# Optimization experiments

Measured on AMD Instinct MI355X. Metric: run time of the kernel, lower is better.

## Reference

```python
import jax, jax.numpy as jnp
import numpy as np

N, K, C_S, C_Z, C_G, H, NUM_RBF = 768, 32, 384, 128, 16, 4, 64
E = N * K
DH = C_Z // H  # 32
LN_EPS = 1e-5
DIST_EPS = 1e-8


def _rbf(D, D_min=0.0, D_max=20.0, D_count=NUM_RBF):
    # Gaussian radial basis expansion (GVP/ProteinMPNN style)
    mu = jnp.linspace(D_min, D_max, D_count, dtype=D.dtype)
    sigma = (D_max - D_min) / D_count
    return jnp.exp(-(((D[..., None] - mu) / sigma) ** 2))


def setup_inputs() -> dict:
    key = jax.random.key(0)
    ks = jax.random.split(key, 24)
    node_features = jax.random.normal(ks[0], (N, C_S), dtype=jnp.float32)
    node_trans = jax.random.uniform(ks[1], (N, 3), dtype=jnp.float32) * 30.0  # coords in a 30A box
    edge_features = jax.random.normal(ks[2], (E, C_Z), dtype=jnp.float32)
    src = jax.random.randint(ks[3], (E,), 0, N)
    dst = jnp.repeat(jnp.arange(N), K)  # sorted-by-destination layout (assume_sorted)
    edge_index = jnp.stack([src, dst]).astype(jnp.int64)

    def lin(k, fan_in, fan_out, scale=0.02):
        return jax.random.normal(k, (fan_in, fan_out), dtype=jnp.float32) * scale

    return {
        "node_features": node_features,
        "node_trans": node_trans,
        "edge_features": edge_features,
        "edge_index": edge_index,
        "w_left": lin(ks[4], C_S, C_G), "b_left": jnp.zeros((C_G,), jnp.float32),
        "w_right": lin(ks[5], C_S, C_G), "b_right": jnp.zeros((C_G,), jnp.float32),
        "w_bgate": lin(ks[6], C_G * C_G, C_Z), "b_bgate": jnp.zeros((C_Z,), jnp.float32),
        "w_dist": lin(ks[7], NUM_RBF, C_Z), "b_dist": jnp.zeros((C_Z,), jnp.float32),
        "w_tobias": lin(ks[8], C_Z, H),
        "ln_g": jnp.ones((C_Z,), jnp.float32), "ln_b": jnp.zeros((C_Z,), jnp.float32),
        "w_q": lin(ks[9], C_Z, C_Z), "b_q": jnp.zeros((C_Z,), jnp.float32),
        "w_kv": lin(ks[10], C_Z, 2 * C_Z), "b_kv": jnp.zeros((2 * C_Z,), jnp.float32),
        "w_out": lin(ks[11], C_Z, C_Z), "b_out": jnp.zeros((C_Z,), jnp.float32),
        "w_ogate": lin(ks[12], C_Z, C_Z), "b_ogate": jnp.zeros((C_Z,), jnp.float32),
    }


def reference(node_features, node_trans, edge_features, edge_index,
              w_left, b_left, w_right, b_right, w_bgate, b_bgate,
              w_dist, b_dist, w_tobias, ln_g, ln_b,
              w_q, b_q, w_kv, b_kv, w_out, b_out, w_ogate, b_ogate):
    # sparse -> knn graph (edges pre-sorted by destination, exactly K per node)
    knn_idx = edge_index[0].reshape(N, K)            # [N, K] source node of each neighbor edge
    feat = edge_features.reshape(N, K, C_Z)          # [N, K, c_z]

    # LayerNorm over c_z
    mu = feat.mean(-1, keepdims=True)
    var = feat.var(-1, keepdims=True)
    z = (feat - mu) * jax.lax.rsqrt(var + LN_EPS) * ln_g + ln_b  # [N, K, c_z]

    # outer-product gating bias
    nl = node_features @ w_left + b_left             # [N, c_gate_s]
    nr = node_features @ w_right + b_right
    e1 = nl[knn_idx]                                 # [N, K, c_gate_s]
    e2 = nr[knn_idx]
    edge3 = jnp.einsum('nik,njl->nijkl', e1, e2).reshape(N, K, K, C_G * C_G)
    gate = edge3 @ w_bgate + b_bgate                 # [N, K, K, c_z]

    # RBF distance bias
    t = node_trans[knn_idx]                          # [N, K, 3]
    diff = t[:, :, None, :] - t[:, None, :, :] + DIST_EPS
    dist = jnp.sqrt(jnp.sum(diff * diff, axis=-1))   # [N, K, K]
    db = _rbf(dist) @ w_dist + b_dist                # [N, K, K, c_z]
    bias = (jax.nn.sigmoid(gate) * db) @ w_tobias    # [N, K, K, H]

    # attention over the K neighbors of each node
    q = (z @ w_q + b_q).reshape(N, K, H, DH)
    kv = z @ w_kv + b_kv
    k_ = kv[..., :C_Z].reshape(N, K, H, DH)
    v = kv[..., C_Z:].reshape(N, K, H, DH)
    scores = jnp.einsum('nihd,njhd->nhij', q, k_) / jnp.sqrt(jnp.asarray(DH, q.dtype))
    scores = scores + bias.transpose(0, 3, 1, 2)     # [N, H, K, K] (mask all-True -> no -inf term)
    p = jax.nn.softmax(scores, axis=-1)
    o = jnp.einsum('nhij,njhd->nihd', p, v).reshape(N, K, C_Z)

    # output gate + projection, then knn -> sparse (identity reshape: full mask, sorted edges)
    o = o * jax.nn.sigmoid(z @ w_ogate + b_ogate)
    out = (o @ w_out + b_out).reshape(E, C_Z)
    return out
```

## Files before the change

### kernel.cpp

```cpp
#include <hip/hip_runtime.h>

#define NN   768
#define KKN  32
#define CS   384
#define CZ   128
#define CG   16
#define NH   4
#define DHD  32
#define NRBF 64
#define EE   (NN*KKN)

#define RBF_STEP    (20.0f/63.0f)
#define RBF_INVSTEP (63.0f/20.0f)
#define RBF_INVSIG  3.2f
#define RBF_SI      (RBF_STEP*RBF_INVSIG)

typedef __attribute__((ext_vector_type(8))) short bf16x8;
typedef __attribute__((ext_vector_type(4))) float f32x4;

__device__ __forceinline__ float bfl(unsigned int u){ return __uint_as_float(u << 16); }
__device__ __forceinline__ float bfh(unsigned int u){ return __uint_as_float(u & 0xFFFF0000u); }
__device__ __forceinline__ unsigned int packbf(float a, float b){
  unsigned int r;
  asm("v_cvt_pk_bf16_f32 %0, %1, %2" : "=v"(r) : "v"(a), "v"(b));
  return r;
}
__device__ __forceinline__ float fastrcp(float x){
  float r;
  asm("v_rcp_f32 %0, %1" : "=v"(r) : "v"(x));
  return r;
}
__device__ __forceinline__ float sigm(float x){ return fastrcp(1.0f + __expf(-x)); }

__global__ __launch_bounds__(256) void k1_pre(
    const float* __restrict__ nf, const float* __restrict__ ef,
    const float* __restrict__ wl, const float* __restrict__ bl,
    const float* __restrict__ wr, const float* __restrict__ br,
    const float* __restrict__ lng, const float* __restrict__ lnb,
    float* __restrict__ nlw, float* __restrict__ nrw,
    unsigned short* __restrict__ zw,
    const float* __restrict__ wq, const float* __restrict__ wkv,
    const float* __restrict__ wog, const float* __restrict__ wout,
    const float* __restrict__ wd, const float* __restrict__ wt,
    const float* __restrict__ wb, const float* __restrict__ bgf,
    unsigned short* __restrict__ wqkvogT, unsigned short* __restrict__ woutT,
    unsigned short* __restrict__ wdT, unsigned short* __restrict__ wtT,
    unsigned short* __restrict__ wbP, unsigned short* __restrict__ bgP)
{
  int b = blockIdx.x, t = threadIdx.x;
  if (b < 1536){
    int rl = t >> 4, l16 = t & 15;
    size_t e = (size_t)b*16 + rl;
    const float4* row = (const float4*)(ef + e*CZ);
    float4 x0 = row[l16*2], x1 = row[l16*2+1];
    float v[8] = {x0.x,x0.y,x0.z,x0.w,x1.x,x1.y,x1.z,x1.w};
    float s = 0.f, q = 0.f;
    #pragma unroll
    for (int u=0;u<8;u++){ s += v[u]; q += v[u]*v[u]; }
    #pragma unroll
    for (int m=1;m<16;m<<=1){ s += __shfl_xor(s,m); q += __shfl_xor(q,m); }
    float mean = s*(1.f/128.f);
    float var  = q*(1.f/128.f) - mean*mean;
    float rs = rsqrtf(var + 1e-5f);
    int c0 = l16*8;
    unsigned int pk[4];
    #pragma unroll
    for (int u=0;u<4;u++){
      float z0 = (v[2*u]  -mean)*rs*lng[c0+2*u]   + lnb[c0+2*u];
      float z1 = (v[2*u+1]-mean)*rs*lng[c0+2*u+1] + lnb[c0+2*u+1];
      pk[u] = packbf(z0,z1);
    }
    ((uint4*)(zw + e*CZ))[l16] = make_uint4(pk[0],pk[1],pk[2],pk[3]);
  } else if (b < 2304){
    int blk2 = b - 1536;
    int seg = blk2 / 96;
    int within = blk2 - seg*96;
    int gid = within*256 + t;
    int side = (gid >= 12288) ? 1 : 0;
    int idx = gid - side*12288;
    int nd = idx >> 4, c = idx & 15;
    const float* w = side ? wr : wl;
    float acc = (seg==0) ? (side ? br[c] : bl[c]) : 0.f;
    const float* nrow = nf + (size_t)nd*CS;
    int kb = seg*48;
    #pragma unroll 4
    for (int k=kb;k<kb+48;k++) acc += nrow[k]*w[k*CG+c];
    atomicAdd((side? nrw : nlw)+idx, acc);
  } else {
    int id = (b - 2304)*256 + t;
    float v[8];
    if (id < 8192){
      int c = id & 511, g = id >> 9;
      const float* src; int ld, col;
      if (c < 128){ src = wq; ld = 128; col = c; }
      else if (c < 384){ src = wkv; ld = 256; col = c-128; }
      else { src = wog; ld = 128; col = c-384; }
      #pragma unroll
      for (int j=0;j<8;j++) v[j] = src[(size_t)(g*8+j)*ld + col];
      *(uint4*)(wqkvogT + c*128 + ((g + c)&15)*8) = make_uint4(
        packbf(v[0],v[1]),packbf(v[2],v[3]),packbf(v[4],v[5]),packbf(v[6],v[7]));
    } else if (id < 10240){
      int l = id - 8192; int c = l & 127, g = l >> 7;
      #pragma unroll
      for (int j=0;j<8;j++) v[j] = wout[(size_t)(g*8+j)*128 + c];
      *(uint4*)(woutT + c*128 + ((g + c)&15)*8) = make_uint4(
        packbf(v[0],v[1]),packbf(v[2],v[3]),packbf(v[4],v[5]),packbf(v[6],v[7]));
    } else if (id < 11392){
      int l = id - 10240; int c = l & 127, g = l >> 7;
      #pragma unroll
      for (int j=0;j<8;j++) v[j] = (g<8) ? wd[(size_t)(g*8+j)*128 + c] : 0.f;
      *(uint4*)(wdT + c*72 + g*8) = make_uint4(
        packbf(v[0],v[1]),packbf(v[2],v[3]),packbf(v[4],v[5]),packbf(v[6],v[7]));
    } else if (id < 11460){
      int l = id - 11392; int h = l / 17, g = l % 17;
      #pragma unroll
      for (int j=0;j<8;j++){ int cc = g*8+j; v[j] = (cc<128)? wt[cc*4 + h] : 0.f; }
      *(uint4*)(wtT + h*136 + g*8) = make_uint4(
        packbf(v[0],v[1]),packbf(v[2],v[3]),packbf(v[4],v[5]),packbf(v[6],v[7]));
    } else if (id < 15556){
      int l2 = id - 11460;
      int c = l2 >> 5, sl = l2 & 31;
      int kl0 = sl*8;
      #pragma unroll
      for (int j=0;j<8;j++) v[j] = wb[(size_t)(kl0+j)*128 + c];
      *(uint4*)(wbP + c*256 + kl0) = make_uint4(
        packbf(v[0],v[1]),packbf(v[2],v[3]),packbf(v[4],v[5]),packbf(v[6],v[7]));
    } else if (id < 15684){
      int c = id - 15556;
      *(uint4*)(bgP + c*8) = make_uint4(packbf(bgf[c], 0.f), 0u, 0u, 0u);
    }
  }
}

__global__ __launch_bounds__(256) void k1b_sprep(
    const float* __restrict__ nlw, const float* __restrict__ nrw,
    const unsigned short* __restrict__ wbP,
    unsigned short* __restrict__ S_all, unsigned short* __restrict__ nrb)
{
  int n = blockIdx.x, t = threadIdx.x;
  float e1[16];
  #pragma unroll
  for (int k=0;k<16;k++) e1[k] = nlw[n*CG + k];
  int c = t>>1, l0 = (t&1)*8;
  float S[8];
  #pragma unroll
  for (int u=0;u<8;u++) S[u]=0.f;
  const unsigned short* wrow = wbP + c*256 + l0;
  #pragma unroll 4
  for (int k=0;k<16;k++){
    uint4 wv = *(const uint4*)(wrow + k*16);
    float wf[8] = { bfl(wv.x), bfh(wv.x), bfl(wv.y), bfh(wv.y),
                    bfl(wv.z), bfh(wv.z), bfl(wv.w), bfh(wv.w) };
    float ev = e1[k];
    #pragma unroll
    for (int u=0;u<8;u++) S[u] = fmaf(ev, wf[u], S[u]);
  }
  *(uint4*)(S_all + (size_t)n*2048 + c*16 + l0) = make_uint4(
    packbf(S[0],S[1]), packbf(S[2],S[3]), packbf(S[4],S[5]), packbf(S[6],S[7]));
  if (t < 8){
    *(unsigned int*)(nrb + n*CG + 2*t) = packbf(nrw[n*CG + 2*t], nrw[n*CG + 2*t + 1]);
  }
}

__global__ __launch_bounds__(256,4) void k2_bias(
    const long long* __restrict__ eidx, const float* __restrict__ trans,
    const unsigned short* __restrict__ S_all, const unsigned short* __restrict__ nrb,
    const unsigned short* __restrict__ wdTg, const unsigned short* __restrict__ wtTg,
    const unsigned short* __restrict__ bgP, const float* __restrict__ bd,
    float* __restrict__ biasw)
{
  int n = blockIdx.x >> 3, chunk = blockIdx.x & 7;
  int i0 = chunk*4;
  int t = threadIdx.x;
  int wave = t>>6, lane = t&63, q = lane>>4, l15 = lane&15;

  __shared__ __align__(16) unsigned short rbfb[32*72];
  __shared__ __align__(16) unsigned short Xb  [32*136];
  __shared__ __align__(16) float t3s[32][4];
  __shared__ __align__(16) float dsm[4][32];
  __shared__ int srcs[32];

  f32x4 zero4 = {0.f,0.f,0.f,0.f};
  uint4 uz = make_uint4(0,0,0,0);

  if (t < 32) srcs[t] = (int)eidx[(size_t)n*KKN + t];
  __syncthreads();
  if (t < 32){ int s = srcs[t];
    t3s[t][0]=trans[s*3]; t3s[t][1]=trans[s*3+1]; t3s[t][2]=trans[s*3+2]; }
  uint4 wdf[2][2];
  #pragma unroll
  for (int mt=0;mt<2;mt++){
    #pragma unroll
    for (int ks=0;ks<2;ks++)
      wdf[mt][ks] = *(const uint4*)(wdTg + (wave*32+mt*16+l15)*72 + ks*32 + q*8);
  }
  uint4 wtf[4];
  #pragma unroll
  for (int ks=0;ks<4;ks++)
    wtf[ks] = *(const uint4*)(wtTg + (l15&3)*136 + ks*32 + q*8);
  uint4 aBias[2];
  #pragma unroll
  for (int mt=0;mt<2;mt++)
    aBias[mt] = (q == 2) ? *(const uint4*)(bgP + (wave*32+mt*16+l15)*8) : uz;
  uint4 bE[2];
  #pragma unroll
  for (int nt=0;nt<2;nt++){
    int jn = srcs[nt*16 + l15];
    bE[nt] = (q < 2) ? *(const uint4*)(nrb + jn*CG + q*8)
                     : (q == 2 ? make_uint4(0x3F80u,0u,0u,0u) : uz);
  }
  uint4 aS[2], aSn[2];
  {
    int s0 = srcs[i0];
    #pragma unroll
    for (int mt=0;mt<2;mt++)
      aS[mt] = (q < 2) ? *(const uint4*)(S_all + (size_t)s0*2048 + (wave*32+mt*16+l15)*16 + q*8)
                       : aBias[mt];
  }
  __syncthreads();
  if (t < 128){
    int ii=t>>5, j=t&31;
    float dx=t3s[i0+ii][0]-t3s[j][0]+1e-8f;
    float dy=t3s[i0+ii][1]-t3s[j][1]+1e-8f;
    float dz=t3s[i0+ii][2]-t3s[j][2]+1e-8f;
    dsm[ii][j]=sqrtf(dx*dx+dy*dy+dz*dz);
  }
  __syncthreads();

  int jr = t>>3, sl = t&7;
  int c0base = wave*32 + q*4;
  float4 bdv[2];
  #pragma unroll
  for (int mt=0;mt<2;mt++) bdv[mt] = *(const float4*)(bd + c0base + mt*16);

  #pragma unroll 1
  for (int ii=0; ii<4; ii++){
    {
      float dI = dsm[ii][jr]*RBF_INVSIG;
      float e[8];
      #pragma unroll
      for (int u=0;u<8;u++){
        float x = fmaf((float)(sl*8+u), -RBF_SI, dI);
        e[u] = __expf(-x*x);
      }
      *(uint4*)&rbfb[jr*72 + sl*8] = make_uint4(
        packbf(e[0],e[1]), packbf(e[2],e[3]), packbf(e[4],e[5]), packbf(e[6],e[7]));
    }
    if (ii < 3){
      int s_n = srcs[i0+ii+1];
      #pragma unroll
      for (int mt=0;mt<2;mt++)
        aSn[mt] = (q < 2) ? *(const uint4*)(S_all + (size_t)s_n*2048 + (wave*32+mt*16+l15)*16 + q*8)
                          : aBias[mt];
    }
    __syncthreads();

    f32x4 ga[2][2], da[2][2];
    #pragma unroll
    for(int a=0;a<2;a++){
      #pragma unroll
      for(int b2=0;b2<2;b2++){ ga[a][b2]=zero4; da[a][b2]=zero4; }
    }
    #pragma unroll
    for(int mt=0;mt<2;mt++){
      #pragma unroll
      for(int nt=0;nt<2;nt++)
        ga[mt][nt] = __builtin_amdgcn_mfma_f32_16x16x32_bf16(
          *(const bf16x8*)&aS[mt], *(const bf16x8*)&bE[nt], ga[mt][nt], 0,0,0);
    }
    #pragma unroll
    for(int ks=0;ks<2;ks++){
      bf16x8 bR[2];
      #pragma unroll
      for(int nt=0;nt<2;nt++) bR[nt] = *(const bf16x8*)&rbfb[(nt*16+l15)*72 + ks*32 + q*8];
      #pragma unroll
      for(int mt=0;mt<2;mt++){
        #pragma unroll
        for(int nt=0;nt<2;nt++)
          da[mt][nt] = __builtin_amdgcn_mfma_f32_16x16x32_bf16(
            *(const bf16x8*)&wdf[mt][ks], bR[nt], da[mt][nt], 0,0,0);
      }
    }
    #pragma unroll
    for(int mt=0;mt<2;mt++){
      int c0 = c0base + mt*16;
      float4 bv = bdv[mt];
      #pragma unroll
      for(int nt=0;nt<2;nt++){
        float x0 = fastrcp(1.f + __expf(-ga[mt][nt][0]))*(da[mt][nt][0]+bv.x);
        float x1 = fastrcp(1.f + __expf(-ga[mt][nt][1]))*(da[mt][nt][1]+bv.y);
        float x2 = fastrcp(1.f + __expf(-ga[mt][nt][2]))*(da[mt][nt][2]+bv.z);
        float x3 = fastrcp(1.f + __expf(-ga[mt][nt][3]))*(da[mt][nt][3]+bv.w);
        *(uint2*)&Xb[(nt*16+l15)*136 + c0] = make_uint2(packbf(x0,x1), packbf(x2,x3));
      }
    }
    __syncthreads();

    if (wave < 2){
      f32x4 bacc = {0.f,0.f,0.f,0.f};
      #pragma unroll
      for(int ks=0;ks<4;ks++){
        bf16x8 bX = *(const bf16x8*)&Xb[(wave*16+l15)*136 + ks*32 + q*8];
        bacc = __builtin_amdgcn_mfma_f32_16x16x32_bf16(*(const bf16x8*)&wtf[ks], bX, bacc, 0,0,0);
      }
      if (q==0){
        int j = wave*16 + l15;
        float* base = biasw + (((size_t)n*4)*32 + (i0+ii))*32 + j;
        base[0] = bacc[0]; base[1024] = bacc[1]; base[2048] = bacc[2]; base[3072] = bacc[3];
      }
    }
    aS[0] = aSn[0]; aS[1] = aSn[1];
  }
}

__global__ __launch_bounds__(256,4) void k3_attn(
    const unsigned short* __restrict__ zw, const float* __restrict__ biasw,
    const unsigned short* __restrict__ wqkvogT, const unsigned short* __restrict__ woutT,
    const float* __restrict__ bq, const float* __restrict__ bkv, const float* __restrict__ bog,
    const float* __restrict__ bout, float* __restrict__ out)
{
  int n = blockIdx.x, t = threadIdx.x;
  int w = t>>6, lane = t&63, q = lane>>4, l15 = lane&15;

  __shared__ __align__(16) char smem[40960];
  f32x4 zero4 = {0.f,0.f,0.f,0.f};

  bf16x8 zfr[2][4];
  #pragma unroll
  for (int nt=0;nt<2;nt++){
    const unsigned short* zr = zw + ((size_t)n*32 + nt*16 + l15)*128;
    #pragma unroll
    for (int ks=0;ks<4;ks++) zfr[nt][ks] = *(const bf16x8*)(zr + ks*32 + q*8);
  }
  const float* bb = biasw + (size_t)(n*4 + w)*1024;
  float bbv[2][4][2];
  #pragma unroll
  for (int mt=0;mt<2;mt++){
    #pragma unroll
    for (int rg=0;rg<4;rg++){
      int i = mt*16 + q*4 + rg;
      bbv[mt][rg][0] = bb[i*32 + l15];
      bbv[mt][rg][1] = bb[i*32 + 16 + l15];
    }
  }
  const float* bseg = (w==0)? bq : (w==1)? bkv : (w==2)? (bkv+128) : bog;

  for (int r=0;r<8;r++){
    float4 bv = *(const float4*)(bseg + r*16 + q*4);
    f32x4 acc0 = zero4, acc1 = zero4;
    int cg = w*128 + r*16 + l15;
    const unsigned short* wrow = wqkvogT + cg*128;
    #pragma unroll
    for (int ks=0;ks<4;ks++){
      bf16x8 af = *(const bf16x8*)(wrow + (((ks*4+q) + cg)&15)*8);
      acc0 = __builtin_amdgcn_mfma_f32_16x16x32_bf16(af, zfr[0][ks], acc0, 0,0,0);
      acc1 = __builtin_amdgcn_mfma_f32_16x16x32_bf16(af, zfr[1][ks], acc1, 0,0,0);
    }
    #pragma unroll
    for (int nt=0;nt<2;nt++){
      f32x4 a = nt? acc1 : acc0;
      float v0,v1,v2,v3;
      if (w==3){ v0=sigm(a[0]+bv.x); v1=sigm(a[1]+bv.y); v2=sigm(a[2]+bv.z); v3=sigm(a[3]+bv.w); }
      else     { v0=a[0]+bv.x; v1=a[1]+bv.y; v2=a[2]+bv.z; v3=a[3]+bv.w; }
      int i = nt*16 + l15;
      if (w==2){
        unsigned short* vt = (unsigned short*)(smem + 16384) + (r*16 + q*4)*32 + i;
        unsigned int u01 = packbf(v0,v1), u23 = packbf(v2,v3);
        vt[0]  = (unsigned short)u01;  vt[32] = (unsigned short)(u01>>16);
        vt[64] = (unsigned short)u23;  vt[96] = (unsigned short)(u23>>16);
      } else {
        int blk = ((r*2 + (q>>1)) + i) & 15;
        *(uint2*)(smem + w*8192 + i*256 + blk*16 + (q&1)*8) = make_uint2(packbf(v0,v1), packbf(v2,v3));
      }
    }
  }
  __syncthreads();

  f32x4 sc4[2][2];
  {
    uint4 aQ[2], bK[2];
    #pragma unroll
    for (int mt=0;mt<2;mt++){
      int row = mt*16 + l15;
      aQ[mt] = *(const uint4*)(smem + row*256 + (((w*4+q) + row)&15)*16);
    }
    #pragma unroll
    for (int nt=0;nt<2;nt++){
      int row = nt*16 + l15;
      bK[nt] = *(const uint4*)(smem + 8192 + row*256 + (((w*4+q) + row)&15)*16);
    }
    #pragma unroll
    for (int mt=0;mt<2;mt++){
      #pragma unroll
      for (int nt=0;nt<2;nt++)
        sc4[mt][nt] = __builtin_amdgcn_mfma_f32_16x16x32_bf16(
          *(const bf16x8*)&aQ[mt], *(const bf16x8*)&bK[nt], zero4, 0,0,0);
    }
  }
  float inv_[2][4];
  #pragma unroll
  for (int mt=0;mt<2;mt++){
    #pragma unroll
    for (int rg=0;rg<4;rg++){
      sc4[mt][0][rg] = fmaf(sc4[mt][0][rg], 0.17677669529663687f, bbv[mt][rg][0]);
      sc4[mt][1][rg] = fmaf(sc4[mt][1][rg], 0.17677669529663687f, bbv[mt][rg][1]);
      float m = fmaxf(sc4[mt][0][rg], sc4[mt][1][rg]);
      m = fmaxf(m, __shfl_xor(m,1));
      m = fmaxf(m, __shfl_xor(m,2));
      m = fmaxf(m, __shfl_xor(m,4));
      m = fmaxf(m, __shfl_xor(m,8));
      sc4[mt][0][rg] = __expf(sc4[mt][0][rg] - m);
      sc4[mt][1][rg] = __expf(sc4[mt][1][rg] - m);
      float s = sc4[mt][0][rg] + sc4[mt][1][rg];
      s += __shfl_xor(s,1); s += __shfl_xor(s,2);
      s += __shfl_xor(s,4); s += __shfl_xor(s,8);
      inv_[mt][rg] = fastrcp(s);
    }
  }
  unsigned short* Pl = (unsigned short*)(smem + 32768 + w*2048);
  #pragma unroll
  for (int mt=0;mt<2;mt++){
    #pragma unroll
    for (int nt=0;nt<2;nt++){
      unsigned int u01 = packbf(sc4[mt][nt][0], sc4[mt][nt][1]);
      unsigned int u23 = packbf(sc4[mt][nt][2], sc4[mt][nt][3]);
      unsigned short* pp = Pl + (mt*16 + q*4)*32 + nt*16 + l15;
      pp[0]  = (unsigned short)u01;  pp[32] = (unsigned short)(u01>>16);
      pp[64] = (unsigned short)u23;  pp[96] = (unsigned short)(u23>>16);
    }
  }
  __syncthreads();

  f32x4 ov[2][2];
  {
    uint4 aP[2], bV[2];
    #pragma unroll
    for (int mt=0;mt<2;mt++)
      aP[mt] = *(const uint4*)(Pl + (mt*16 + l15)*32 + q*8);
    #pragma unroll
    for (int nt2=0;nt2<2;nt2++)
      bV[nt2] = *(const uint4*)((unsigned short*)(smem + 16384) + (w*32 + nt2*16 + l15)*32 + q*8);
    #pragma unroll
    for (int mt=0;mt<2;mt++){
      #pragma unroll
      for (int nt2=0;nt2<2;nt2++)
        ov[mt][nt2] = __builtin_amdgcn_mfma_f32_16x16x32_bf16(
          *(const bf16x8*)&aP[mt], *(const bf16x8*)&bV[nt2], zero4, 0,0,0);
    }
  }
  #pragma unroll
  for (int mt=0;mt<2;mt++){
    #pragma unroll
    for (int nt2=0;nt2<2;nt2++){
      #pragma unroll
      for (int rg=0;rg<4;rg++){
        int i = mt*16 + q*4 + rg;
        int c = w*32 + nt2*16 + l15;
        int off = i*256 + (((c>>3) + i)&15)*16 + (c&7)*2;
        unsigned short gus = *(const unsigned short*)(smem + 24576 + off);
        float g = __uint_as_float(((unsigned int)gus) << 16);
        float yv = ov[mt][nt2][rg] * inv_[mt][rg] * g;
        *(unsigned short*)(smem + off) = (unsigned short)packbf(yv, yv);
      }
    }
  }
  __syncthreads();

  bf16x8 yfr[2][4];
  #pragma unroll
  for (int mt=0;mt<2;mt++){
    int row = mt*16 + l15;
    #pragma unroll
    for (int ks=0;ks<4;ks++)
      yfr[mt][ks] = *(const bf16x8*)(smem + row*256 + (((ks*4+q) + row)&15)*16);
  }
  #pragma unroll
  for (int r2=0;r2<2;r2++){
    int c0 = (r2*4 + w)*16;
    int cg2 = c0 + l15;
    const unsigned short* orow = woutT + cg2*128;
    f32x4 oa0 = zero4, oa1 = zero4;
    #pragma unroll
    for (int ks=0;ks<4;ks++){
      bf16x8 bf = *(const bf16x8*)(orow + (((ks*4+q) + cg2)&15)*8);
      oa0 = __builtin_amdgcn_mfma_f32_16x16x32_bf16(yfr[0][ks], bf, oa0, 0,0,0);
      oa1 = __builtin_amdgcn_mfma_f32_16x16x32_bf16(yfr[1][ks], bf, oa1, 0,0,0);
    }
    float bov = bout[cg2];
    #pragma unroll
    for (int mt=0;mt<2;mt++){
      f32x4 oa = mt? oa1 : oa0;
      #pragma unroll
      for (int rg=0; rg<4; rg++){
        int i = mt*16 + q*4 + rg;
        out[((size_t)n*32 + i)*128 + cg2] = oa[rg] + bov;
      }
    }
  }
}

extern "C" void kernel_launch(void* const* d_in, const int* in_sizes, int n_in,
                              void* d_out, int out_size, void* d_ws, size_t ws_size,
                              hipStream_t stream)
{
  const float* nf  = (const float*)d_in[0];
  const float* tr  = (const float*)d_in[1];
  const float* ef  = (const float*)d_in[2];
  const long long* ei = (const long long*)d_in[3];
  const float* wl  = (const float*)d_in[4];  const float* bl  = (const float*)d_in[5];
  const float* wr  = (const float*)d_in[6];  const float* br  = (const float*)d_in[7];
  const float* wbg = (const float*)d_in[8];  const float* bbg = (const float*)d_in[9];
  const float* wdi = (const float*)d_in[10]; const float* bdi = (const float*)d_in[11];
  const float* wtb = (const float*)d_in[12];
  const float* lng = (const float*)d_in[13]; const float* lnb = (const float*)d_in[14];
  const float* wq  = (const float*)d_in[15]; const float* bq  = (const float*)d_in[16];
  const float* wkv = (const float*)d_in[17]; const float* bkv = (const float*)d_in[18];
  const float* wo  = (const float*)d_in[19]; const float* bo  = (const float*)d_in[20];
  const float* wog = (const float*)d_in[21]; const float* bog = (const float*)d_in[22];
  float* outp = (float*)d_out;
  float* ws = (float*)d_ws;
  float* nlw = ws;
  float* nrw = ws + 12288;
  float* biasw = ws + 24576;
  unsigned short* zw      = (unsigned short*)(ws + 3170304);
  unsigned short* wqkvogT = (unsigned short*)(ws + 4743168);
  unsigned short* woutT   = (unsigned short*)(ws + 4775936);
  unsigned short* wdTg    = (unsigned short*)(ws + 4784128);
  unsigned short* wtTg    = (unsigned short*)(ws + 4788736);
  unsigned short* bgPg    = wtTg + 544;
  unsigned short* wbPg    = (unsigned short*)(ws + 4789824);
  unsigned short* S_all   = (unsigned short*)(ws + 4806208);
  unsigned short* nrb     = (unsigned short*)(ws + 5592640);

  hipMemsetAsync(nlw, 0, 24576*sizeof(float), stream);
  hipLaunchKernelGGL(k1_pre, dim3(2366), dim3(256), 0, stream,
                     nf, ef, wl, bl, wr, br, lng, lnb, nlw, nrw, zw,
                     wq, wkv, wog, wo, wdi, wtb, wbg, bbg,
                     wqkvogT, woutT, wdTg, wtTg, wbPg, bgPg);
  hipLaunchKernelGGL(k1b_sprep, dim3(768), dim3(256), 0, stream,
                     nlw, nrw, wbPg, S_all, nrb);
  hipLaunchKernelGGL(k2_bias, dim3(6144), dim3(256), 0, stream,
                     ei, tr, S_all, nrb, wdTg, wtTg, bgPg, bdi, biasw);
  hipLaunchKernelGGL(k3_attn, dim3(768), dim3(256), 0, stream,
                     zw, biasw, wqkvogT, woutT, bq, bkv, bog, bo, outp);
}
```

Baseline: 192.9 us.

## Fuse bias computation kernel into attention kernel, keep bias in shared memory

```diff
diff --git a/kernel.cpp b/kernel.cpp
--- a/kernel.cpp
+++ b/kernel.cpp
@@ -162,23 +162,27 @@
   }
 }
 
-__global__ __launch_bounds__(256,4) void k2_bias(
+__global__ __launch_bounds__(256,4) void k23_fused(
     const long long* __restrict__ eidx, const float* __restrict__ trans,
     const unsigned short* __restrict__ S_all, const unsigned short* __restrict__ nrb,
     const unsigned short* __restrict__ wdTg, const unsigned short* __restrict__ wtTg,
     const unsigned short* __restrict__ bgP, const float* __restrict__ bd,
-    float* __restrict__ biasw)
+    const unsigned short* __restrict__ zw,
+    const unsigned short* __restrict__ wqkvogT, const unsigned short* __restrict__ woutT,
+    const float* __restrict__ bq, const float* __restrict__ bkv, const float* __restrict__ bog,
+    const float* __restrict__ bout, float* __restrict__ out)
 {
-  int n = blockIdx.x >> 3, chunk = blockIdx.x & 7;
-  int i0 = chunk*4;
-  int t = threadIdx.x;
+  int n = blockIdx.x, t = threadIdx.x;
   int wave = t>>6, lane = t&63, q = lane>>4, l15 = lane&15;
-
-  __shared__ __align__(16) unsigned short rbfb[32*72];
-  __shared__ __align__(16) unsigned short Xb  [32*136];
-  __shared__ __align__(16) float t3s[32][4];
-  __shared__ __align__(16) float dsm[4][32];
-  __shared__ int srcs[32];
+  int w = wave;
+
+  __shared__ __align__(16) char smem[40960];
+  float* biasF          = (float*)smem;
+  unsigned short* Xb    = (unsigned short*)(smem + 16384);
+  unsigned short* rbfb  = (unsigned short*)(smem + 25088);
+  float* dsm            = (float*)(smem + 29696);
+  float* t3s            = (float*)(smem + 33792);
+  int*   srcs           = (int*)(smem + 34304);
 
   f32x4 zero4 = {0.f,0.f,0.f,0.f};
   uint4 uz = make_uint4(0,0,0,0);
@@ -186,7 +190,7 @@
   if (t < 32) srcs[t] = (int)eidx[(size_t)n*KKN + t];
   __syncthreads();
   if (t < 32){ int s = srcs[t];
-    t3s[t][0]=trans[s*3]; t3s[t][1]=trans[s*3+1]; t3s[t][2]=trans[s*3+2]; }
+    t3s[t*4]=trans[s*3]; t3s[t*4+1]=trans[s*3+1]; t3s[t*4+2]=trans[s*3+2]; }
   uint4 wdf[2][2];
   #pragma unroll
   for (int mt=0;mt<2;mt++){
@@ -211,19 +215,21 @@
   }
   uint4 aS[2], aSn[2];
   {
-    int s0 = srcs[i0];
+    int s0 = srcs[0];
     #pragma unroll
     for (int mt=0;mt<2;mt++)
       aS[mt] = (q < 2) ? *(const uint4*)(S_all + (size_t)s0*2048 + (wave*32+mt*16+l15)*16 + q*8)
                        : aBias[mt];
   }
   __syncthreads();
-  if (t < 128){
-    int ii=t>>5, j=t&31;
-    float dx=t3s[i0+ii][0]-t3s[j][0]+1e-8f;
-    float dy=t3s[i0+ii][1]-t3s[j][1]+1e-8f;
-    float dz=t3s[i0+ii][2]-t3s[j][2]+1e-8f;
-    dsm[ii][j]=sqrtf(dx*dx+dy*dy+dz*dz);
+  #pragma unroll
+  for (int u=0;u<4;u++){
+    int idx = t + u*256;
+    int di = idx >> 5, j = idx & 31;
+    float dx=t3s[di*4]  -t3s[j*4]  +1e-8f;
+    float dy=t3s[di*4+1]-t3s[j*4+1]+1e-8f;
+    float dz=t3s[di*4+2]-t3s[j*4+2]+1e-8f;
+    dsm[di*32+j]=sqrtf(dx*dx+dy*dy+dz*dz);
   }
   __syncthreads();
 
@@ -234,9 +240,9 @@
   for (int mt=0;mt<2;mt++) bdv[mt] = *(const float4*)(bd + c0base + mt*16);
 
   #pragma unroll 1
-  for (int ii=0; ii<4; ii++){
+  for (int ii=0; ii<32; ii++){
     {
-      float dI = dsm[ii][jr]*RBF_INVSIG;
+      float dI = dsm[ii*32 + jr]*RBF_INVSIG;
       float e[8];
       #pragma unroll
       for (int u=0;u<8;u++){
@@ -246,8 +252,8 @@
       *(uint4*)&rbfb[jr*72 + sl*8] = make_uint4(
         packbf(e[0],e[1]), packbf(e[2],e[3]), packbf(e[4],e[5]), packbf(e[6],e[7]));
     }
-    if (ii < 3){
-      int s_n = srcs[i0+ii+1];
+    if (ii < 31){
+      int s_n = srcs[ii+1];
       #pragma unroll
       for (int mt=0;mt<2;mt++)
         aSn[mt] = (q < 2) ? *(const uint4*)(S_all + (size_t)s_n*2048 + (wave*32+mt*16+l15)*16 + q*8)
@@ -305,26 +311,27 @@
       }
       if (q==0){
         int j = wave*16 + l15;
-        float* base = biasw + (((size_t)n*4)*32 + (i0+ii))*32 + j;
+        float* base = biasF + ii*32 + j;
         base[0] = bacc[0]; base[1024] = bacc[1]; base[2048] = bacc[2]; base[3072] = bacc[3];
       }
     }
     aS[0] = aSn[0]; aS[1] = aSn[1];
   }
-}
-
-__global__ __launch_bounds__(256,4) void k3_attn(
-    const unsigned short* __restrict__ zw, const float* __restrict__ biasw,
-    const unsigned short* __restrict__ wqkvogT, const unsigned short* __restrict__ woutT,
-    const float* __restrict__ bq, const float* __restrict__ bkv, const float* __restrict__ bog,
-    const float* __restrict__ bout, float* __restrict__ out)
-{
-  int n = blockIdx.x, t = threadIdx.x;
-  int w = t>>6, lane = t&63, q = lane>>4, l15 = lane&15;
-
-  __shared__ __align__(16) char smem[40960];
-  f32x4 zero4 = {0.f,0.f,0.f,0.f};
-
+  __syncthreads();
+
+  float bbv[2][4][2];
+  {
+    const float* bbl = biasF + w*1024;
+    #pragma unroll
+    for (int mt=0;mt<2;mt++){
+      #pragma unroll
+      for (int rg=0;rg<4;rg++){
+        int i = mt*16 + q*4 + rg;
+        bbv[mt][rg][0] = bbl[i*32 + l15];
+        bbv[mt][rg][1] = bbl[i*32 + 16 + l15];
+      }
+    }
+  }
   bf16x8 zfr[2][4];
   #pragma unroll
   for (int nt=0;nt<2;nt++){
@@ -332,18 +339,8 @@
     #pragma unroll
     for (int ks=0;ks<4;ks++) zfr[nt][ks] = *(const bf16x8*)(zr + ks*32 + q*8);
   }
-  const float* bb = biasw + (size_t)(n*4 + w)*1024;
-  float bbv[2][4][2];
-  #pragma unroll
-  for (int mt=0;mt<2;mt++){
-    #pragma unroll
-    for (int rg=0;rg<4;rg++){
-      int i = mt*16 + q*4 + rg;
-      bbv[mt][rg][0] = bb[i*32 + l15];
-      bbv[mt][rg][1] = bb[i*32 + 16 + l15];
-    }
-  }
   const float* bseg = (w==0)? bq : (w==1)? bkv : (w==2)? (bkv+128) : bog;
+  __syncthreads();
 
   for (int r=0;r<8;r++){
     float4 bv = *(const float4*)(bseg + r*16 + q*4);
@@ -521,7 +518,6 @@
   float* ws = (float*)d_ws;
   float* nlw = ws;
   float* nrw = ws + 12288;
-  float* biasw = ws + 24576;
   unsigned short* zw      = (unsigned short*)(ws + 3170304);
   unsigned short* wqkvogT = (unsigned short*)(ws + 4743168);
   unsigned short* woutT   = (unsigned short*)(ws + 4775936);
@@ -539,8 +535,7 @@
                      wqkvogT, woutT, wdTg, wtTg, wbPg, bgPg);
   hipLaunchKernelGGL(k1b_sprep, dim3(768), dim3(256), 0, stream,
                      nlw, nrw, wbPg, S_all, nrb);
-  hipLaunchKernelGGL(k2_bias, dim3(6144), dim3(256), 0, stream,
-                     ei, tr, S_all, nrb, wdTg, wtTg, bgPg, bdi, biasw);
-  hipLaunchKernelGGL(k3_attn, dim3(768), dim3(256), 0, stream,
-                     zw, biasw, wqkvogT, woutT, bq, bkv, bog, bo, outp);
+  hipLaunchKernelGGL(k23_fused, dim3(768), dim3(256), 0, stream,
+                     ei, tr, S_all, nrb, wdTg, wtTg, bgPg, bdi,
+                     zw, wqkvogT, woutT, bq, bkv, bog, bo, outp);
 }
```

After: 188.0 us, median of 2. 1.03x faster.
